# Kernel optimization log

Hardware: AMD Instinct MI355X
Metric: run time of the kernel (lower is better)

Reference implementation:

```python
import jax, jax.numpy as jnp
import numpy as np

B, T, C = 4, 2048, 1024
N_HEAD = 16
HS = C // N_HEAD  # head_size = 64


def setup_inputs() -> dict:
    key = jax.random.key(0)
    k1, k2, k3 = jax.random.split(key, 3)
    x = jax.random.normal(k1, (B, T, C), dtype=jnp.float32)
    # torch Linear(in, out, bias=False); stored here as (in, out) so y = x @ W
    W_attn = jax.random.normal(k2, (C, 3 * C), dtype=jnp.float32) * (C ** -0.5)
    W_proj = jax.random.normal(k3, (C, C), dtype=jnp.float32) * (C ** -0.5)
    return {"x": x, "W_attn": W_attn, "W_proj": W_proj}


def reference(x, W_attn, W_proj):
    Bq, Tq, Cq = x.shape
    qkv = x @ W_attn                              # (B, T, 3C)
    q, k, v = jnp.split(qkv, 3, axis=-1)          # each (B, T, C)
    # (B, T, C) -> (B, H, T, hs)
    q = q.reshape(Bq, Tq, N_HEAD, HS).transpose(0, 2, 1, 3)
    k = k.reshape(Bq, Tq, N_HEAD, HS).transpose(0, 2, 1, 3)
    v = v.reshape(Bq, Tq, N_HEAD, HS).transpose(0, 2, 1, 3)
    scale = HS ** -0.5
    att = jnp.einsum("bhqd,bhkd->bhqk", q, k) * scale  # (B, H, T, T)
    causal = jnp.tril(jnp.ones((Tq, Tq), dtype=bool))
    att = jnp.where(causal[None, None], att, jnp.finfo(att.dtype).min)
    att = jax.nn.softmax(att, axis=-1)
    y = jnp.einsum("bhqk,bhkd->bhqd", att, v)     # (B, H, T, hs)
    y = y.transpose(0, 2, 1, 3).reshape(Bq, Tq, Cq)
    return y @ W_proj                             # (B, T, C)
```

## Files before the change

### kernel.cpp

```cpp
#include <hip/hip_runtime.h>
#include <stdint.h>

typedef __bf16 bf16x8 __attribute__((ext_vector_type(8)));
typedef float f32x4 __attribute__((ext_vector_type(4)));

__device__ __forceinline__ unsigned short f2bf(float f) {
  unsigned u = __builtin_bit_cast(unsigned, f);
  u = (u + 0x7fffu + ((u >> 16) & 1u)) >> 16;
  return (unsigned short)u;
}

__device__ __forceinline__ unsigned cvt_pk_bf16(float a, float b) {
  unsigned r;
  asm("v_cvt_pk_bf16_f32 %0, %1, %2" : "=v"(r) : "v"(a), "v"(b));
  return r;
}

__device__ __forceinline__ void gload_lds16(const unsigned short* g, unsigned short* l) {
  __builtin_amdgcn_global_load_lds(
      (__attribute__((address_space(1))) unsigned int*)g,
      (__attribute__((address_space(3))) unsigned int*)l, 16, 0, 0);
}

__device__ __forceinline__ void store_val(float* p, float v) { *p = v; }
__device__ __forceinline__ void store_val(unsigned short* p, float v) { *p = f2bf(v); }

__global__ __launch_bounds__(256) void f2bf_kernel(const float* __restrict__ in,
                                                   unsigned short* __restrict__ out, int n) {
  int stride = gridDim.x * blockDim.x * 4;
  for (int i = (blockIdx.x * blockDim.x + threadIdx.x) * 4; i < n; i += stride) {
    float4 v = *(const float4*)(in + i);
    ushort4 o;
    o.x = f2bf(v.x); o.y = f2bf(v.y); o.z = f2bf(v.z); o.w = f2bf(v.w);
    *(ushort4*)(out + i) = o;
  }
}

__global__ __launch_bounds__(256) void transpose_f2bf(const float* __restrict__ in,
                                                      unsigned short* __restrict__ out,
                                                      int R, int Ccols, float qscale, int qcols) {
  __shared__ unsigned short t[64][65];
  int r0 = blockIdx.y * 64, c0 = blockIdx.x * 64;
  int tid = threadIdx.x;
#pragma unroll
  for (int rep = 0; rep < 16; rep++) {
    int idx = rep * 256 + tid;
    int rr = idx >> 6, cc = idx & 63;
    float v = in[(size_t)(r0 + rr) * Ccols + c0 + cc];
    if (c0 + cc < qcols) v *= qscale;
    t[rr][cc] = f2bf(v);
  }
  __syncthreads();
#pragma unroll
  for (int rep = 0; rep < 16; rep++) {
    int idx = rep * 256 + tid;
    int cc = idx >> 6, rr = idx & 63;
    out[(size_t)(c0 + cc) * R + r0 + rr] = t[rr][cc];
  }
}

__global__ __launch_bounds__(256) void make_vt(const unsigned short* __restrict__ qkv,
                                               unsigned short* __restrict__ vt) {
  __shared__ unsigned short t[64][65];
  int bh = blockIdx.x;
  int b = bh >> 4, h = bh & 15;
  int t0 = blockIdx.y * 64;
  int tid = threadIdx.x;
#pragma unroll
  for (int rep = 0; rep < 16; rep++) {
    int idx = rep * 256 + tid;
    int tt = idx >> 6, dd = idx & 63;
    t[tt][dd] = qkv[(size_t)(b * 2048 + t0 + tt) * 3072 + 2048 + h * 64 + dd];
  }
  __syncthreads();
#pragma unroll
  for (int rep = 0; rep < 16; rep++) {
    int idx = rep * 256 + tid;
    int dd = idx >> 6, tt = idx & 63;
    vt[(size_t)bh * 131072 + (size_t)dd * 2048 + t0 + tt] = t[tt][dd];
  }
}

template <typename OutT>
__global__ __launch_bounds__(512, 2) void gemm_bt(const unsigned short* __restrict__ A,
                                                  const unsigned short* __restrict__ Bt,
                                                  OutT* __restrict__ C, int M, int N, int K,
                                                  int mtiles) {
  __shared__ unsigned short lds3[3][24576];
  const int tid = threadIdx.x;
  const int wid = tid >> 6, l = tid & 63;
  const int wm = wid >> 2, wn = wid & 3;
  const int lr = l & 15, lg = l >> 4;

  int nwg = gridDim.x;
  int q8 = nwg >> 3;
  int bid = blockIdx.x;
  int bs = (bid & 7) * q8 + (bid >> 3);
  int mt = bs % mtiles, nt = bs / mtiles;
  const int m0 = mt * 128, n0 = nt * 256;

  const int srow = tid >> 3;
  const int schunk = ((tid & 7) ^ (srow & 7)) * 8;
  const unsigned short* gA0 = A + (size_t)(m0 + srow) * K + schunk;
  const unsigned short* gB0 = Bt + (size_t)(n0 + srow) * K + schunk;
  const int wslice = wid * 512;

  int arow[4], brow[2][2], xoff[2];
#pragma unroll
  for (int m = 0; m < 4; m++) arow[m] = (wm * 64 + m * 16 + lr) * 64;
#pragma unroll
  for (int qq = 0; qq < 2; qq++)
#pragma unroll
    for (int j = 0; j < 2; j++) brow[qq][j] = 8192 + (wn * 64 + qq * 32 + j * 16 + lr) * 64;
#pragma unroll
  for (int ks = 0; ks < 2; ks++) xoff[ks] = ((ks * 4 + lg) ^ (lr & 7)) * 8;

  f32x4 acc[4][4] = {};
  const int NT = K >> 6;

  gload_lds16(gA0, &lds3[0][wslice]);
  gload_lds16(gA0 + (size_t)64 * K, &lds3[0][4096 + wslice]);
#pragma unroll
  for (int u = 0; u < 4; u++)
    gload_lds16(gB0 + (size_t)(u * 64) * K, &lds3[0][8192 + u * 4096 + wslice]);
  gload_lds16(gA0 + 64, &lds3[1][wslice]);
  gload_lds16(gA0 + (size_t)64 * K + 64, &lds3[1][4096 + wslice]);
#pragma unroll
  for (int u = 0; u < 4; u++)
    gload_lds16(gB0 + (size_t)(u * 64) * K + 64, &lds3[1][8192 + u * 4096 + wslice]);

  int cb = 0;
  for (int t = 0; t < NT; t++) {
    if (t == NT - 1) {
      asm volatile("s_waitcnt vmcnt(0)" ::: "memory");
    } else {
      asm volatile("s_waitcnt vmcnt(6)" ::: "memory");
    }
    __builtin_amdgcn_s_barrier();
    const unsigned short* bufc = lds3[cb];
    int pb = cb + 2; if (pb >= 3) pb -= 3;
    unsigned short* bufp = lds3[pb];
    const int k2 = (t + 2) * 64;
    const bool pre = (t + 2) < NT;

    if (pre) {
      gload_lds16(gA0 + k2, bufp + wslice);
      gload_lds16(gA0 + (size_t)64 * K + k2, bufp + 4096 + wslice);
      gload_lds16(gB0 + k2, bufp + 8192 + wslice);
    }
    bf16x8 af[4][2];
#pragma unroll
    for (int m = 0; m < 4; m++)
#pragma unroll
      for (int ks = 0; ks < 2; ks++)
        af[m][ks] = *(const bf16x8*)&bufc[arow[m] + xoff[ks]];
    {
      bf16x8 bq[2][2];
#pragma unroll
      for (int j = 0; j < 2; j++)
#pragma unroll
        for (int ks = 0; ks < 2; ks++)
          bq[j][ks] = *(const bf16x8*)&bufc[brow[0][j] + xoff[ks]];
      __builtin_amdgcn_s_setprio(1);
#pragma unroll
      for (int m = 0; m < 4; m++)
#pragma unroll
        for (int j = 0; j < 2; j++)
#pragma unroll
          for (int ks = 0; ks < 2; ks++)
            acc[m][j] = __builtin_amdgcn_mfma_f32_16x16x32_bf16(af[m][ks], bq[j][ks], acc[m][j], 0, 0, 0);
      __builtin_amdgcn_s_setprio(0);
    }
    if (pre) {
      gload_lds16(gB0 + (size_t)64 * K + k2, bufp + 12288 + wslice);
      gload_lds16(gB0 + (size_t)128 * K + k2, bufp + 16384 + wslice);
      gload_lds16(gB0 + (size_t)192 * K + k2, bufp + 20480 + wslice);
    }
    {
      bf16x8 bq[2][2];
#pragma unroll
      for (int j = 0; j < 2; j++)
#pragma unroll
        for (int ks = 0; ks < 2; ks++)
          bq[j][ks] = *(const bf16x8*)&bufc[brow[1][j] + xoff[ks]];
      __builtin_amdgcn_s_setprio(1);
#pragma unroll
      for (int m = 0; m < 4; m++)
#pragma unroll
        for (int j = 0; j < 2; j++)
#pragma unroll
          for (int ks = 0; ks < 2; ks++)
            acc[m][2 + j] = __builtin_amdgcn_mfma_f32_16x16x32_bf16(af[m][ks], bq[j][ks], acc[m][2 + j], 0, 0, 0);
      __builtin_amdgcn_s_setprio(0);
    }
    cb = (cb == 2) ? 0 : cb + 1;
  }

#pragma unroll
  for (int m = 0; m < 4; m++)
#pragma unroll
    for (int n = 0; n < 4; n++)
#pragma unroll
      for (int i = 0; i < 4; i++) {
        size_t row = (size_t)(m0 + wm * 64 + m * 16 + lg * 4 + i);
        size_t col = (size_t)(n0 + wn * 64 + n * 16 + lr);
        store_val(&C[row * N + col], acc[m][n][i]);
      }
}

__global__ __launch_bounds__(256, 3) void attn_kernel(const unsigned short* __restrict__ qkv,
                                                      const unsigned short* __restrict__ vt,
                                                      unsigned short* __restrict__ y) {
  __shared__ unsigned short k_lds[2][64 * 64];
  __shared__ unsigned short v_lds[2][64 * 64];
  __shared__ unsigned short p_lds[8][16 * 64];
  int tid = threadIdx.x;
  int w = tid >> 6, l = tid & 63;
  int lr = l & 15, lg = l >> 4;
  int g4 = lg * 4;
  int lband = l & 48;
  int bh = blockIdx.x;
  int b = bh >> 4, h = bh & 15;
  int qgrp = 15 - blockIdx.y;
  int q0 = qgrp * 128 + w * 32;

  char* plo = (char*)p_lds[w * 2];
  char* phi = (char*)p_lds[w * 2 + 1];

  int srow = tid >> 3;
  int schunk = (tid & 7) ^ (srow & 7);
  const unsigned short* gK0 = qkv + (size_t)(b * 2048 + srow) * 3072 + 1024 + h * 64 + schunk * 8;
  const unsigned short* gK1 = gK0 + (size_t)32 * 3072;
  const unsigned short* gV0 = vt + (size_t)bh * 131072 + (size_t)srow * 2048 + schunk * 8;
  const unsigned short* gV1 = gV0 + (size_t)32 * 2048;
  int ldsbase0 = w * 512;
  int ldsbase1 = 2048 + w * 512;

  const unsigned short* qp = qkv + (size_t)(b * 2048 + q0 + lr) * 3072 + h * 64 + lg * 8;
  bf16x8 aQ0lo = *(const bf16x8*)qp;
  bf16x8 aQ1lo = *(const bf16x8*)(qp + 32);
  bf16x8 aQ0hi = *(const bf16x8*)(qp + 16 * 3072);
  bf16x8 aQ1hi = *(const bf16x8*)(qp + 16 * 3072 + 32);

  f32x4 Olo[4] = {}, Ohi[4] = {};
  float mlo = -3.0e38f, mhi = -3.0e38f;
  float sumlo = 0.f, sumhi = 0.f;

  int rx = lr & 7;
  int kc0 = (lg ^ rx) * 8;
  int kc1 = ((4 + lg) ^ rx) * 8;

  int nbmax = ((qgrp * 128 + 96) >> 6) + 1;
  int kend = q0 + 31;
  int kdiag = q0 >> 6;

  gload_lds16(gK0, &k_lds[0][ldsbase0]);
  gload_lds16(gK1, &k_lds[0][ldsbase1]);
  gload_lds16(gV0, &v_lds[0][ldsbase0]);
  gload_lds16(gV1, &v_lds[0][ldsbase1]);
  __syncthreads();

  int cur = 0;
  for (int kb = 0; kb < nbmax; kb++) {
    int kbase = kb * 64;
    if (kb + 1 < nbmax) {
      size_t koff = (size_t)(kbase + 64) * 3072;
      size_t voff = (size_t)(kbase + 64);
      int nxt = cur ^ 1;
      gload_lds16(gK0 + koff, &k_lds[nxt][ldsbase0]);
      gload_lds16(gK1 + koff, &k_lds[nxt][ldsbase1]);
      gload_lds16(gV0 + voff, &v_lds[nxt][ldsbase0]);
      gload_lds16(gV1 + voff, &v_lds[nxt][ldsbase1]);
    }
    if (kbase <= kend) {
      const unsigned short* kl = k_lds[cur];
      const unsigned short* vl = v_lds[cur];
      f32x4 svlo[4], svhi[4];
      __builtin_amdgcn_s_setprio(1);
#pragma unroll
      for (int n = 0; n < 4; n++) {
        bf16x8 kf0 = *(const bf16x8*)&kl[(n * 16 + lr) * 64 + kc0];
        bf16x8 kf1 = *(const bf16x8*)&kl[(n * 16 + lr) * 64 + kc1];
        f32x4 z = {};
        z = __builtin_amdgcn_mfma_f32_16x16x32_bf16(kf0, aQ0lo, z, 0, 0, 0);
        z = __builtin_amdgcn_mfma_f32_16x16x32_bf16(kf1, aQ1lo, z, 0, 0, 0);
        svlo[n] = z;
        f32x4 z2 = {};
        z2 = __builtin_amdgcn_mfma_f32_16x16x32_bf16(kf0, aQ0hi, z2, 0, 0, 0);
        z2 = __builtin_amdgcn_mfma_f32_16x16x32_bf16(kf1, aQ1hi, z2, 0, 0, 0);
        svhi[n] = z2;
      }
      __builtin_amdgcn_s_setprio(0);
      if (kb == kdiag) {
#pragma unroll
        for (int n = 0; n < 4; n++)
#pragma unroll
          for (int i = 0; i < 4; i++) {
            int kk = kbase + n * 16 + g4 + i;
            if (kk > q0 + lr) svlo[n][i] = -1.0e38f;
            if (kk > q0 + 16 + lr) svhi[n][i] = -1.0e38f;
          }
      }
      float tmlo = fmaxf(
          fmaxf(fmaxf(fmaxf(svlo[0][0], svlo[0][1]), fmaxf(svlo[0][2], svlo[0][3])),
                fmaxf(fmaxf(svlo[1][0], svlo[1][1]), fmaxf(svlo[1][2], svlo[1][3]))),
          fmaxf(fmaxf(fmaxf(svlo[2][0], svlo[2][1]), fmaxf(svlo[2][2], svlo[2][3])),
                fmaxf(fmaxf(svlo[3][0], svlo[3][1]), fmaxf(svlo[3][2], svlo[3][3]))));
      float tmhi = fmaxf(
          fmaxf(fmaxf(fmaxf(svhi[0][0], svhi[0][1]), fmaxf(svhi[0][2], svhi[0][3])),
                fmaxf(fmaxf(svhi[1][0], svhi[1][1]), fmaxf(svhi[1][2], svhi[1][3]))),
          fmaxf(fmaxf(fmaxf(svhi[2][0], svhi[2][1]), fmaxf(svhi[2][2], svhi[2][3])),
                fmaxf(fmaxf(svhi[3][0], svhi[3][1]), fmaxf(svhi[3][2], svhi[3][3]))));
      tmlo = fmaxf(tmlo, __shfl_xor(tmlo, 16));
      tmlo = fmaxf(tmlo, __shfl_xor(tmlo, 32));
      tmhi = fmaxf(tmhi, __shfl_xor(tmhi, 16));
      tmhi = fmaxf(tmhi, __shfl_xor(tmhi, 32));
      if (__any(tmlo > mlo + 11.54f || tmhi > mhi + 11.54f)) {
        float mnlo = fmaxf(mlo, tmlo), mnhi = fmaxf(mhi, tmhi);
        float faclo = __builtin_amdgcn_exp2f(mlo - mnlo);
        float fachi = __builtin_amdgcn_exp2f(mhi - mnhi);
        mlo = mnlo; mhi = mnhi;
        sumlo *= faclo; sumhi *= fachi;
        float f0 = __shfl(faclo, lband | g4);
        float f1 = __shfl(faclo, lband | (g4 + 1));
        float f2 = __shfl(faclo, lband | (g4 + 2));
        float f3 = __shfl(faclo, lband | (g4 + 3));
        float h0 = __shfl(fachi, lband | g4);
        float h1 = __shfl(fachi, lband | (g4 + 1));
        float h2 = __shfl(fachi, lband | (g4 + 2));
        float h3 = __shfl(fachi, lband | (g4 + 3));
#pragma unroll
        for (int n2 = 0; n2 < 4; n2++) {
          Olo[n2][0] *= f0; Olo[n2][1] *= f1; Olo[n2][2] *= f2; Olo[n2][3] *= f3;
          Ohi[n2][0] *= h0; Ohi[n2][1] *= h1; Ohi[n2][2] *= h2; Ohi[n2][3] *= h3;
        }
      }
      float pslo = 0.f, pshi = 0.f;
      unsigned pk0lo[4], pk1lo[4], pk0hi[4], pk1hi[4];
#pragma unroll
      for (int n = 0; n < 4; n++) {
        float a0 = __builtin_amdgcn_exp2f(svlo[n][0] - mlo);
        float a1 = __builtin_amdgcn_exp2f(svlo[n][1] - mlo);
        float a2 = __builtin_amdgcn_exp2f(svlo[n][2] - mlo);
        float a3 = __builtin_amdgcn_exp2f(svlo[n][3] - mlo);
        pslo += (a0 + a1) + (a2 + a3);
        pk0lo[n] = cvt_pk_bf16(a0, a1);
        pk1lo[n] = cvt_pk_bf16(a2, a3);
        float c0 = __builtin_amdgcn_exp2f(svhi[n][0] - mhi);
        float c1 = __builtin_amdgcn_exp2f(svhi[n][1] - mhi);
        float c2 = __builtin_amdgcn_exp2f(svhi[n][2] - mhi);
        float c3 = __builtin_amdgcn_exp2f(svhi[n][3] - mhi);
        pshi += (c0 + c1) + (c2 + c3);
        pk0hi[n] = cvt_pk_bf16(c0, c1);
        pk1hi[n] = cvt_pk_bf16(c2, c3);
      }
      pslo += __shfl_xor(pslo, 16);
      pslo += __shfl_xor(pslo, 32);
      pshi += __shfl_xor(pshi, 16);
      pshi += __shfl_xor(pshi, 32);
      sumlo += pslo;
      sumhi += pshi;
#pragma unroll
      for (int n = 0; n < 4; n++) {
        int chunk = (2 * n + (lg >> 1)) ^ rx;
        int off = lr * 128 + chunk * 16 + (lg & 1) * 8;
        *(uint2*)(plo + off) = make_uint2(pk0lo[n], pk1lo[n]);
        *(uint2*)(phi + off) = make_uint2(pk0hi[n], pk1hi[n]);
      }
      bf16x8 aPlo0 = *(const bf16x8*)(plo + lr * 128 + (lg ^ rx) * 16);
      bf16x8 aPlo1 = *(const bf16x8*)(plo + lr * 128 + ((4 + lg) ^ rx) * 16);
      bf16x8 aPhi0 = *(const bf16x8*)(phi + lr * 128 + (lg ^ rx) * 16);
      bf16x8 aPhi1 = *(const bf16x8*)(phi + lr * 128 + ((4 + lg) ^ rx) * 16);
      __builtin_amdgcn_s_setprio(1);
#pragma unroll
      for (int n2 = 0; n2 < 4; n2++) {
        bf16x8 v0 = *(const bf16x8*)&vl[(n2 * 16 + lr) * 64 + kc0];
        bf16x8 v1 = *(const bf16x8*)&vl[(n2 * 16 + lr) * 64 + kc1];
        Olo[n2] = __builtin_amdgcn_mfma_f32_16x16x32_bf16(aPlo0, v0, Olo[n2], 0, 0, 0);
        Olo[n2] = __builtin_amdgcn_mfma_f32_16x16x32_bf16(aPlo1, v1, Olo[n2], 0, 0, 0);
        Ohi[n2] = __builtin_amdgcn_mfma_f32_16x16x32_bf16(aPhi0, v0, Ohi[n2], 0, 0, 0);
        Ohi[n2] = __builtin_amdgcn_mfma_f32_16x16x32_bf16(aPhi1, v1, Ohi[n2], 0, 0, 0);
      }
      __builtin_amdgcn_s_setprio(0);
    }
    __syncthreads();
    cur ^= 1;
  }
  float s0 = __shfl(sumlo, lband | g4);
  float s1 = __shfl(sumlo, lband | (g4 + 1));
  float s2 = __shfl(sumlo, lband | (g4 + 2));
  float s3 = __shfl(sumlo, lband | (g4 + 3));
  float t0 = __shfl(sumhi, lband | g4);
  float t1 = __shfl(sumhi, lband | (g4 + 1));
  float t2 = __shfl(sumhi, lband | (g4 + 2));
  float t3 = __shfl(sumhi, lband | (g4 + 3));
  float rl0 = 1.f / s0, rl1 = 1.f / s1, rl2 = 1.f / s2, rl3 = 1.f / s3;
  float rh0 = 1.f / t0, rh1 = 1.f / t1, rh2 = 1.f / t2, rh3 = 1.f / t3;
#pragma unroll
  for (int n2 = 0; n2 < 4; n2++) {
    size_t base = (size_t)(b * 2048 + q0 + g4) * 1024 + h * 64 + n2 * 16 + lr;
    y[base] = f2bf(Olo[n2][0] * rl0);
    y[base + 1024] = f2bf(Olo[n2][1] * rl1);
    y[base + 2048] = f2bf(Olo[n2][2] * rl2);
    y[base + 3072] = f2bf(Olo[n2][3] * rl3);
    size_t bhh = base + (size_t)16 * 1024;
    y[bhh] = f2bf(Ohi[n2][0] * rh0);
    y[bhh + 1024] = f2bf(Ohi[n2][1] * rh1);
    y[bhh + 2048] = f2bf(Ohi[n2][2] * rh2);
    y[bhh + 3072] = f2bf(Ohi[n2][3] * rh3);
  }
}

extern "C" void kernel_launch(void* const* d_in, const int* in_sizes, int n_in,
                              void* d_out, int out_size, void* d_ws, size_t ws_size,
                              hipStream_t stream) {
  const float* x = (const float*)d_in[0];
  const float* Wa = (const float*)d_in[1];
  const float* Wp = (const float*)d_in[2];
  float* out = (float*)d_out;

  char* ws = (char*)d_ws;
  size_t off = 0;
  unsigned short* xb = (unsigned short*)(ws + off);   off += (size_t)8192 * 1024 * 2;
  unsigned short* Wta = (unsigned short*)(ws + off);  off += (size_t)3072 * 1024 * 2;
  unsigned short* Wtp = (unsigned short*)(ws + off);  off += (size_t)1024 * 1024 * 2;
  unsigned short* qkvb = (unsigned short*)(ws + off); off += (size_t)8192 * 3072 * 2;
  unsigned short* vtb = (unsigned short*)(ws + off);  off += (size_t)64 * 64 * 2048 * 2;
  unsigned short* yb = (unsigned short*)(ws + off);   off += (size_t)8192 * 1024 * 2;

  const float SC = 0.125f * 1.44269504f;
  f2bf_kernel<<<2048, 256, 0, stream>>>(x, xb, 8192 * 1024);
  transpose_f2bf<<<dim3(48, 16), 256, 0, stream>>>(Wa, Wta, 1024, 3072, SC, 1024);
  transpose_f2bf<<<dim3(16, 16), 256, 0, stream>>>(Wp, Wtp, 1024, 1024, 1.0f, 0);
  gemm_bt<unsigned short><<<768, 512, 0, stream>>>(xb, Wta, qkvb, 8192, 3072, 1024, 64);
  make_vt<<<dim3(64, 32), 256, 0, stream>>>(qkvb, vtb);
  attn_kernel<<<dim3(64, 16), 256, 0, stream>>>(qkvb, vtb, yb);
  gemm_bt<float><<<256, 512, 0, stream>>>(yb, Wtp, out, 8192, 1024, 1024, 64);
}
```

Before: 172.8 us.

## Halve P staging LDS per wave and raise attention occupancy to four blocks

```diff
diff --git a/kernel.cpp b/kernel.cpp
--- a/kernel.cpp
+++ b/kernel.cpp
@@ -208,12 +208,12 @@
       }
 }
 
-__global__ __launch_bounds__(256, 3) void attn_kernel(const unsigned short* __restrict__ qkv,
+__global__ __launch_bounds__(256, 4) void attn_kernel(const unsigned short* __restrict__ qkv,
                                                       const unsigned short* __restrict__ vt,
                                                       unsigned short* __restrict__ y) {
   __shared__ unsigned short k_lds[2][64 * 64];
   __shared__ unsigned short v_lds[2][64 * 64];
-  __shared__ unsigned short p_lds[8][16 * 64];
+  __shared__ unsigned short p_lds[4][16 * 64];
   int tid = threadIdx.x;
   int w = tid >> 6, l = tid & 63;
   int lr = l & 15, lg = l >> 4;
@@ -224,8 +224,7 @@
   int qgrp = 15 - blockIdx.y;
   int q0 = qgrp * 128 + w * 32;
 
-  char* plo = (char*)p_lds[w * 2];
-  char* phi = (char*)p_lds[w * 2 + 1];
+  char* pstrip = (char*)p_lds[w];
 
   int srow = tid >> 3;
   int schunk = (tid & 7) ^ (srow & 7);
@@ -301,16 +300,18 @@
             if (kk > q0 + 16 + lr) svhi[n][i] = -1.0e38f;
           }
       }
-      float tmlo = fmaxf(
-          fmaxf(fmaxf(fmaxf(svlo[0][0], svlo[0][1]), fmaxf(svlo[0][2], svlo[0][3])),
-                fmaxf(fmaxf(svlo[1][0], svlo[1][1]), fmaxf(svlo[1][2], svlo[1][3]))),
-          fmaxf(fmaxf(fmaxf(svlo[2][0], svlo[2][1]), fmaxf(svlo[2][2], svlo[2][3])),
-                fmaxf(fmaxf(svlo[3][0], svlo[3][1]), fmaxf(svlo[3][2], svlo[3][3]))));
-      float tmhi = fmaxf(
-          fmaxf(fmaxf(fmaxf(svhi[0][0], svhi[0][1]), fmaxf(svhi[0][2], svhi[0][3])),
-                fmaxf(fmaxf(svhi[1][0], svhi[1][1]), fmaxf(svhi[1][2], svhi[1][3]))),
-          fmaxf(fmaxf(fmaxf(svhi[2][0], svhi[2][1]), fmaxf(svhi[2][2], svhi[2][3])),
-                fmaxf(fmaxf(svhi[3][0], svhi[3][1]), fmaxf(svhi[3][2], svhi[3][3]))));
+      float u0 = fmaxf(fmaxf(svlo[0][0], svlo[0][1]), svlo[0][2]);
+      float u1 = fmaxf(fmaxf(svlo[0][3], svlo[1][0]), svlo[1][1]);
+      float u2 = fmaxf(fmaxf(svlo[1][2], svlo[1][3]), svlo[2][0]);
+      float u3 = fmaxf(fmaxf(svlo[2][1], svlo[2][2]), svlo[2][3]);
+      float u4 = fmaxf(fmaxf(svlo[3][0], svlo[3][1]), svlo[3][2]);
+      float tmlo = fmaxf(fmaxf(fmaxf(u0, u1), u2), fmaxf(fmaxf(u3, u4), svlo[3][3]));
+      float w0 = fmaxf(fmaxf(svhi[0][0], svhi[0][1]), svhi[0][2]);
+      float w1 = fmaxf(fmaxf(svhi[0][3], svhi[1][0]), svhi[1][1]);
+      float w2 = fmaxf(fmaxf(svhi[1][2], svhi[1][3]), svhi[2][0]);
+      float w3 = fmaxf(fmaxf(svhi[2][1], svhi[2][2]), svhi[2][3]);
+      float w4 = fmaxf(fmaxf(svhi[3][0], svhi[3][1]), svhi[3][2]);
+      float tmhi = fmaxf(fmaxf(fmaxf(w0, w1), w2), fmaxf(fmaxf(w3, w4), svhi[3][3]));
       tmlo = fmaxf(tmlo, __shfl_xor(tmlo, 16));
       tmlo = fmaxf(tmlo, __shfl_xor(tmlo, 32));
       tmhi = fmaxf(tmhi, __shfl_xor(tmhi, 16));
@@ -360,26 +361,38 @@
       pshi += __shfl_xor(pshi, 32);
       sumlo += pslo;
       sumhi += pshi;
+      bf16x8 vf0[4], vf1[4];
+#pragma unroll
+      for (int n2 = 0; n2 < 4; n2++) {
+        vf0[n2] = *(const bf16x8*)&vl[(n2 * 16 + lr) * 64 + kc0];
+        vf1[n2] = *(const bf16x8*)&vl[(n2 * 16 + lr) * 64 + kc1];
+      }
 #pragma unroll
       for (int n = 0; n < 4; n++) {
         int chunk = (2 * n + (lg >> 1)) ^ rx;
-        int off = lr * 128 + chunk * 16 + (lg & 1) * 8;
-        *(uint2*)(plo + off) = make_uint2(pk0lo[n], pk1lo[n]);
-        *(uint2*)(phi + off) = make_uint2(pk0hi[n], pk1hi[n]);
-      }
-      bf16x8 aPlo0 = *(const bf16x8*)(plo + lr * 128 + (lg ^ rx) * 16);
-      bf16x8 aPlo1 = *(const bf16x8*)(plo + lr * 128 + ((4 + lg) ^ rx) * 16);
-      bf16x8 aPhi0 = *(const bf16x8*)(phi + lr * 128 + (lg ^ rx) * 16);
-      bf16x8 aPhi1 = *(const bf16x8*)(phi + lr * 128 + ((4 + lg) ^ rx) * 16);
+        *(uint2*)(pstrip + lr * 128 + chunk * 16 + (lg & 1) * 8) = make_uint2(pk0lo[n], pk1lo[n]);
+      }
+      bf16x8 aP0 = *(const bf16x8*)(pstrip + lr * 128 + (lg ^ rx) * 16);
+      bf16x8 aP1 = *(const bf16x8*)(pstrip + lr * 128 + ((4 + lg) ^ rx) * 16);
       __builtin_amdgcn_s_setprio(1);
 #pragma unroll
       for (int n2 = 0; n2 < 4; n2++) {
-        bf16x8 v0 = *(const bf16x8*)&vl[(n2 * 16 + lr) * 64 + kc0];
-        bf16x8 v1 = *(const bf16x8*)&vl[(n2 * 16 + lr) * 64 + kc1];
-        Olo[n2] = __builtin_amdgcn_mfma_f32_16x16x32_bf16(aPlo0, v0, Olo[n2], 0, 0, 0);
-        Olo[n2] = __builtin_amdgcn_mfma_f32_16x16x32_bf16(aPlo1, v1, Olo[n2], 0, 0, 0);
-        Ohi[n2] = __builtin_amdgcn_mfma_f32_16x16x32_bf16(aPhi0, v0, Ohi[n2], 0, 0, 0);
-        Ohi[n2] = __builtin_amdgcn_mfma_f32_16x16x32_bf16(aPhi1, v1, Ohi[n2], 0, 0, 0);
+        Olo[n2] = __builtin_amdgcn_mfma_f32_16x16x32_bf16(aP0, vf0[n2], Olo[n2], 0, 0, 0);
+        Olo[n2] = __builtin_amdgcn_mfma_f32_16x16x32_bf16(aP1, vf1[n2], Olo[n2], 0, 0, 0);
+      }
+      __builtin_amdgcn_s_setprio(0);
+#pragma unroll
+      for (int n = 0; n < 4; n++) {
+        int chunk = (2 * n + (lg >> 1)) ^ rx;
+        *(uint2*)(pstrip + lr * 128 + chunk * 16 + (lg & 1) * 8) = make_uint2(pk0hi[n], pk1hi[n]);
+      }
+      bf16x8 aP2 = *(const bf16x8*)(pstrip + lr * 128 + (lg ^ rx) * 16);
+      bf16x8 aP3 = *(const bf16x8*)(pstrip + lr * 128 + ((4 + lg) ^ rx) * 16);
+      __builtin_amdgcn_s_setprio(1);
+#pragma unroll
+      for (int n2 = 0; n2 < 4; n2++) {
+        Ohi[n2] = __builtin_amdgcn_mfma_f32_16x16x32_bf16(aP2, vf0[n2], Ohi[n2], 0, 0, 0);
+        Ohi[n2] = __builtin_amdgcn_mfma_f32_16x16x32_bf16(aP3, vf1[n2], Ohi[n2], 0, 0, 0);
       }
       __builtin_amdgcn_s_setprio(0);
     }
```

Result: no change. 173.8 us (+0.5%).
